# Optimization experiments

Hardware: AMD Instinct MI355X
Metric: run time of the kernel (lower is better)

Reference implementation:

```python
import jax, jax.numpy as jnp
import numpy as np

# ConvVAE2d config: img_size=64, kernel=stride=16 (same-padding -> 0 pad), non-overlapping patches
BS, CH, IMG, K, NC, HID, LAT = 1024, 3, 64, 16, 10, 1024, 128
OH = IMG // K          # patches per side = 4
L = OH * OH            # patches per image = 16
PD = CH * K * K        # flattened patch dim = 768


def setup_inputs() -> dict:
    key = jax.random.key(0)
    ks = jax.random.split(key, 8)
    def w(k_, shape, fan_in):
        return jax.random.normal(k_, shape, dtype=jnp.float32) * np.float32(1.0 / np.sqrt(fan_in))
    return {
        "x": jax.random.uniform(ks[0], (BS, CH, IMG, IMG), dtype=jnp.float32),
        "c": jax.random.uniform(ks[1], (BS, NC), dtype=jnp.float32),
        # cvae_small.encode params: [patch++class] -> hidden -> 2*latent
        "enc_w1": w(ks[2], (PD + NC, HID), PD + NC),
        "enc_b1": jnp.zeros((HID,), jnp.float32),
        "enc_w2": w(ks[3], (HID, 2 * LAT), HID),
        "enc_b2": jnp.zeros((2 * LAT,), jnp.float32),
        # cvae_small.decode params: [z++class] -> hidden -> patch (sigmoid)
        "dec_w1": w(ks[4], (LAT + NC, HID), LAT + NC),
        "dec_b1": jnp.zeros((HID,), jnp.float32),
        "dec_w2": w(ks[5], (HID, PD), HID),
        "dec_b2": jnp.zeros((PD,), jnp.float32),
    }


def reference(x, c, enc_w1, enc_b1, enc_w2, enc_b2, dec_w1, dec_b1, dec_w2, dec_b2):
    bs = x.shape[0]
    # --- encode_vae_layer: unfold into [bs, L, ch*k*k] patches (stride=k, pad=0) ---
    p = x.reshape(bs, CH, OH, K, OH, K).transpose(0, 2, 4, 1, 3, 5).reshape(bs, L, PD)
    cb = jnp.broadcast_to(c[:, None, :], (bs, L, NC))  # class vector per patch
    h = jax.nn.relu(jnp.concatenate([p, cb], axis=-1) @ enc_w1 + enc_b1)
    mu_logvar = h @ enc_w2 + enc_b2                    # [bs, L, 2*LAT]
    # --- reparameterize_vae_layer (deterministic=True -> z = mu) ---
    mu = mu_logvar[..., :LAT]
    # --- decode_vae_layer: per-patch decode, then fold back (non-overlapping) ---
    hd = jax.nn.relu(jnp.concatenate([mu, cb], axis=-1) @ dec_w1 + dec_b1)
    patches = jax.nn.sigmoid(hd @ dec_w2 + dec_b2)     # [bs, L, PD]
    recon = (patches.reshape(bs, OH, OH, CH, K, K)
                     .transpose(0, 3, 1, 4, 2, 5)
                     .reshape(bs, CH, IMG, IMG))
    # mu_logvar as a [bs, 2*latent, h/stride, w/stride] feature map
    mu_logvar_2d = mu_logvar.transpose(0, 2, 1).reshape(bs, 2 * LAT, OH, OH)
    return recon, mu_logvar_2d
```

## Files before the change

kernel.cpp:

```cpp
#include <hip/hip_runtime.h>

typedef unsigned short u16;
typedef unsigned int   u32;
typedef __bf16 bf16x8 __attribute__((ext_vector_type(8)));
typedef float  f32x4  __attribute__((ext_vector_type(4)));

__device__ __forceinline__ u16 f2b(float f) {
  u32 u = __builtin_bit_cast(u32, f);
  u = (u + 0x7fffu + ((u >> 16) & 1u)) >> 16;
  return (u16)u;
}
__device__ __forceinline__ float b2f(u16 h) {
  u32 u = ((u32)h) << 16;
  return __builtin_bit_cast(float, u);
}
__device__ __forceinline__ float ld_in(const void* p, size_t idx, int isf32) {
  return isf32 ? ((const float*)p)[idx] : b2f(((const u16*)p)[idx]);
}
__device__ __forceinline__ void async_cp16(const u16* g, u16* l) {
  __builtin_amdgcn_global_load_lds(
      (const __attribute__((address_space(1))) void*)g,
      (__attribute__((address_space(3))) void*)l, 16, 0, 0);
}

#define RECON_ELEMS 12582912

__global__ __launch_bounds__(256) void detect_f32(const u16* __restrict__ x,
                                                  int* __restrict__ flag) {
  __shared__ int s;
  if (threadIdx.x == 0) s = 0;
  __syncthreads();
  int bad = 0;
  for (int i = threadIdx.x; i < 2048; i += 256) {
    u16 u = x[i];
    if ((u & 0x8000u) || (u > 0x3F80u)) bad = 1;
  }
  if (bad) atomicOr(&s, 1);
  __syncthreads();
  if (threadIdx.x == 0) *flag = s;
}

__global__ __launch_bounds__(256) void build_a1(const void* __restrict__ x,
                                                const void* __restrict__ c,
                                                u16* __restrict__ A1,
                                                int R, int rowOff,
                                                const int* __restrict__ flag) {
  int g = blockIdx.x * 256 + threadIdx.x;
  if (g >= R * 112) return;
  int row = g / 112, grp = g - row * 112;
  int grow = row + rowOff;
  int b = grow >> 4, l = grow & 15, oh = l >> 2, ow = l & 3;
  int isf = *flag;
  u16* dst = &A1[(size_t)row * 896 + grp * 8];
  int col0 = grp * 8;
  if (col0 < 768) {
    int ch = col0 >> 8, kh = (col0 >> 4) & 15, kw = col0 & 15;
    size_t off = (size_t)b * 12288 + ch * 4096 + (oh * 16 + kh) * 64 + ow * 16 + kw;
    if (isf) {
      const float* s = (const float*)x + off;
      float4 f0 = *(const float4*)(s);
      float4 f1 = *(const float4*)(s + 4);
      dst[0] = f2b(f0.x); dst[1] = f2b(f0.y); dst[2] = f2b(f0.z); dst[3] = f2b(f0.w);
      dst[4] = f2b(f1.x); dst[5] = f2b(f1.y); dst[6] = f2b(f1.z); dst[7] = f2b(f1.w);
    } else {
      *(int4*)dst = *(const int4*)((const u16*)x + off);
    }
  } else {
#pragma unroll
    for (int t = 0; t < 8; ++t) {
      int col = col0 + t;
      dst[t] = (col < 778) ? f2b(ld_in(c, (size_t)b * 10 + (col - 768), isf)) : (u16)0;
    }
  }
}

__global__ __launch_bounds__(256) void prep_weights(const void* __restrict__ ew1,
                                                    const void* __restrict__ ew2,
                                                    const void* __restrict__ dw1,
                                                    const void* __restrict__ dw2,
                                                    u16* __restrict__ W1t,
                                                    u16* __restrict__ EW2t,
                                                    u16* __restrict__ W3t,
                                                    u16* __restrict__ DW2t,
                                                    const int* __restrict__ flag) {
  const int z = blockIdx.z;
  const void* src; u16* dst; int N, Kpad, Ksrc;
  if (z == 0)      { src = ew1; dst = W1t;  N = 1024; Kpad = 896;  Ksrc = 778;  }
  else if (z == 1) { src = ew2; dst = EW2t; N = 256;  Kpad = 1024; Ksrc = 1024; }
  else if (z == 2) { src = dw1; dst = W3t;  N = 1024; Kpad = 160;  Ksrc = 138;  }
  else             { src = dw2; dst = DW2t; N = 768;  Kpad = 1024; Ksrc = 1024; }
  const int k0 = blockIdx.x * 32, n0 = blockIdx.y * 32;
  if (k0 >= Kpad || n0 >= N) return;
  __shared__ float t[32][33];
  const int tx = threadIdx.x & 31, ty = threadIdx.x >> 5;
  const int isf = *flag;
#pragma unroll
  for (int j = 0; j < 4; ++j) {
    int k = k0 + ty + j * 8;
    t[ty + j * 8][tx] = (k < Ksrc) ? ld_in(src, (size_t)k * N + n0 + tx, isf) : 0.0f;
  }
  __syncthreads();
#pragma unroll
  for (int j = 0; j < 4; ++j) {
    int n = n0 + ty + j * 8;
    dst[(size_t)n * Kpad + k0 + tx] = f2b(t[tx][ty + j * 8]);
  }
}

template <int EPI>
__global__ __launch_bounds__(512, 2) void gemm_r3(const u16* __restrict__ A,
                                                  const u16* __restrict__ Bt,
                                                  const void* __restrict__ bias,
                                                  u16* __restrict__ outb,
                                                  float* __restrict__ outf,
                                                  int N, int K, int NBX, int NBY,
                                                  int rowOff,
                                                  const int* __restrict__ flag) {
  extern __shared__ __align__(16) u16 lds[];
  const int bid = blockIdx.x;
  const int xcd = bid & 7, idx = bid >> 3;
  const int byl = idx / NBX;
  const int by = xcd * (NBY >> 3) + byl;
  const int bx = idx - byl * NBX;
  const int rowBase = by * 256, colBase = bx * 256;

  const int tid = threadIdx.x;
  const int lane = tid & 63, w = tid >> 6;
  const int l16 = lane & 15, quad = lane >> 4;
  const int wm = w >> 2, wn = w & 3;
  const int swq = quad ^ ((l16 >> 1) & 3);

  const int isf = *flag;
  float bv[4];
#pragma unroll
  for (int nr = 0; nr < 4; ++nr)
    bv[nr] = ld_in(bias, colBase + wn * 64 + nr * 16 + l16, isf);
  asm volatile("s_waitcnt vmcnt(0)" ::: "memory");

  const int sA0 = tid, sA1 = tid + 512;
  const int rA0 = sA0 >> 2, qA0 = (sA0 & 3) ^ ((rA0 >> 1) & 3);
  const int rA1 = sA1 >> 2, qA1 = (sA1 & 3) ^ ((rA1 >> 1) & 3);
  const u16* gA0 = A  + (size_t)(rowBase + rA0) * K + qA0 * 8;
  const u16* gA1 = A  + (size_t)(rowBase + rA1) * K + qA1 * 8;
  const u16* gB0 = Bt + (size_t)(colBase + rA0) * K + qA0 * 8;
  const u16* gB1 = Bt + (size_t)(colBase + rA1) * K + qA1 * 8;

  f32x4 acc[8][4] = {};
  bf16x8 a[8], b[4];
  const int NT = K >> 5;

  async_cp16(gA0, lds + tid * 8);
  async_cp16(gA1, lds + 4096 + tid * 8);
  async_cp16(gB0, lds + 8192 + tid * 8);
  async_cp16(gB1, lds + 12288 + tid * 8);
  if (NT > 1) {
    u16* D = lds + 16384;
    async_cp16(gA0 + 32, D + tid * 8);
    async_cp16(gA1 + 32, D + 4096 + tid * 8);
    async_cp16(gB0 + 32, D + 8192 + tid * 8);
    async_cp16(gB1 + 32, D + 12288 + tid * 8);
    asm volatile("s_waitcnt vmcnt(4)" ::: "memory");
  } else {
    asm volatile("s_waitcnt vmcnt(0)" ::: "memory");
  }
  __builtin_amdgcn_s_barrier();

  int cur = 0;
  for (int t = 0; t < NT; ++t) {
    const u16* Lq = lds + cur * 16384;
#pragma unroll
    for (int mr = 0; mr < 8; ++mr)
      a[mr] = *(const bf16x8*)(Lq + (wm * 128 + mr * 16 + l16) * 32 + swq * 8);
#pragma unroll
    for (int nr = 0; nr < 4; ++nr)
      b[nr] = *(const bf16x8*)(Lq + 8192 + (wn * 64 + nr * 16 + l16) * 32 + swq * 8);
    if (t + 2 < NT) {
      const int d2 = (cur >= 1) ? cur - 1 : 2;
      u16* D = lds + d2 * 16384;
      const int ko = (t + 2) * 32;
      async_cp16(gA0 + ko, D + tid * 8);
      async_cp16(gA1 + ko, D + 4096 + tid * 8);
      async_cp16(gB0 + ko, D + 8192 + tid * 8);
      async_cp16(gB1 + ko, D + 12288 + tid * 8);
    }
    asm volatile("s_waitcnt lgkmcnt(0)" ::: "memory");
    __builtin_amdgcn_sched_barrier(0);
    __builtin_amdgcn_s_setprio(1);
#pragma unroll
    for (int mr = 0; mr < 8; ++mr)
#pragma unroll
      for (int nr = 0; nr < 4; ++nr)
        acc[mr][nr] = __builtin_amdgcn_mfma_f32_16x16x32_bf16(a[mr], b[nr], acc[mr][nr], 0, 0, 0);
    __builtin_amdgcn_s_setprio(0);
    __builtin_amdgcn_sched_barrier(0);
    if (t + 2 < NT)      asm volatile("s_waitcnt vmcnt(4)" ::: "memory");
    else if (t + 1 < NT) asm volatile("s_waitcnt vmcnt(0)" ::: "memory");
    if (t + 1 < NT) __builtin_amdgcn_s_barrier();
    cur = (cur >= 2) ? 0 : cur + 1;
  }

#pragma unroll
  for (int mr = 0; mr < 8; ++mr) {
    const int row0 = rowBase + wm * 128 + mr * 16 + quad * 4;
#pragma unroll
    for (int nr = 0; nr < 4; ++nr) {
      const int col = colBase + wn * 64 + nr * 16 + l16;
#pragma unroll
      for (int r = 0; r < 4; ++r) {
        const int row = row0 + r;
        float v = acc[mr][nr][r] + bv[nr];
        if (EPI == 0) {
          v = fmaxf(v, 0.0f);
          outb[(size_t)row * N + col] = f2b(v);
        } else {
          v = 1.0f / (1.0f + __expf(-v));
          const int grow = row + rowOff;
          const int bb = grow >> 4, l = grow & 15;
          const int oh = l >> 2, ow = l & 3;
          const int ch = col >> 8, kh = (col >> 4) & 15, kw = col & 15;
          outf[(size_t)bb * 12288 + ch * 4096 + (oh * 16 + kh) * 64 + ow * 16 + kw] = v;
        }
      }
    }
  }
}

__global__ __launch_bounds__(512, 2) void gemm_mid(u16* hio,
    const u16* __restrict__ EW2t, const u16* __restrict__ W3t,
    const void* __restrict__ c, const void* __restrict__ eb2,
    const void* __restrict__ db1, float* __restrict__ out2,
    int rowOff, const int* __restrict__ flag) {
  extern __shared__ __align__(16) u16 lds[];
  const int bid = blockIdx.x;
  const int lrowBase = bid * 64;
  const int growBase = rowOff + lrowBase;
  const int tid = threadIdx.x;
  const int lane = tid & 63, w = tid >> 6;
  const int l16 = lane & 15, quad = lane >> 4;
  const int swq = quad ^ ((l16 >> 1) & 3);
  const int wm = w >> 2, wn4 = w & 3;

  const int isf = *flag;
  float bv2[2], bv3[8][2];
#pragma unroll
  for (int nr = 0; nr < 2; ++nr)
    bv2[nr] = ld_in(eb2, w * 32 + nr * 16 + l16, isf);
#pragma unroll
  for (int np = 0; np < 8; ++np)
#pragma unroll
    for (int nr = 0; nr < 2; ++nr)
      bv3[np][nr] = ld_in(db1, np * 128 + wn4 * 32 + nr * 16 + l16, isf);
  asm volatile("s_waitcnt vmcnt(0)" ::: "memory");

  const int rA = tid >> 3, rcA = tid & 7;
  const int gcA = (rcA & 4) | ((rcA & 3) ^ ((rA >> 1) & 3));
  const u16* gAe = hio + (size_t)(lrowBase + rA) * 1024 + gcA * 8;
  const u16* gBe[4];
#pragma unroll
  for (int j = 0; j < 4; ++j) {
    const int sb = tid + j * 512;
    const int rB = sb >> 3, rcB = sb & 7;
    const int gcB = (rcB & 4) | ((rcB & 3) ^ ((rB >> 1) & 3));
    gBe[j] = EW2t + (size_t)rB * 1024 + gcB * 8;
  }

#define STGE(tt, s) do {                                                   \
    async_cp16(gAe + (tt) * 64, lds + (s) * 4096 + tid * 8);               \
    _Pragma("unroll") for (int j = 0; j < 4; ++j)                          \
      async_cp16(gBe[j] + (tt) * 64,                                       \
                 lds + 8192 + (s) * 16384 + (tid + j * 512) * 8);          \
  } while (0)

  f32x4 acce[4][2] = {};
  STGE(0, 0);
  int p = 0;
  for (int t = 0; t < 16; ++t) {
    if (t + 1 < 16) {
      STGE(t + 1, p ^ 1);
      asm volatile("s_waitcnt vmcnt(5)\n\ts_barrier" ::: "memory");
    } else {
      asm volatile("s_waitcnt vmcnt(0)\n\ts_barrier" ::: "memory");
    }
    const u16* AE = lds + p * 4096;
    const u16* BE = lds + 8192 + p * 16384;
    bf16x8 ae[4][2], be[2][2];
#pragma unroll
    for (int mr = 0; mr < 4; ++mr)
#pragma unroll
      for (int ks = 0; ks < 2; ++ks)
        ae[mr][ks] = *(const bf16x8*)(AE + (mr * 16 + l16) * 64 + ((ks * 4) | swq) * 8);
#pragma unroll
    for (int nr = 0; nr < 2; ++nr)
#pragma unroll
      for (int ks = 0; ks < 2; ++ks)
        be[nr][ks] = *(const bf16x8*)(BE + (w * 32 + nr * 16 + l16) * 64 + ((ks * 4) | swq) * 8);
    asm volatile("s_waitcnt lgkmcnt(0)" ::: "memory");
    __builtin_amdgcn_sched_barrier(0);
    __builtin_amdgcn_s_setprio(1);
#pragma unroll
    for (int mr = 0; mr < 4; ++mr)
#pragma unroll
      for (int nr = 0; nr < 2; ++nr)
#pragma unroll
        for (int ks = 0; ks < 2; ++ks)
          acce[mr][nr] = __builtin_amdgcn_mfma_f32_16x16x32_bf16(ae[mr][ks], be[nr][ks], acce[mr][nr], 0, 0, 0);
    __builtin_amdgcn_s_setprio(0);
    __builtin_amdgcn_sched_barrier(0);
    __builtin_amdgcn_s_barrier();
    p ^= 1;
  }
#undef STGE

  u16* A3 = lds + 40960;
#pragma unroll
  for (int mr = 0; mr < 4; ++mr)
#pragma unroll
    for (int nr = 0; nr < 2; ++nr) {
      const int col = w * 32 + nr * 16 + l16;
      const int row0 = mr * 16 + quad * 4;
#pragma unroll
      for (int r = 0; r < 4; ++r) {
        const int row = row0 + r;
        const int grow = growBase + row;
        const float v = acce[mr][nr][r] + bv2[nr];
        out2[(size_t)(grow >> 4) * 4096 + col * 16 + (grow & 15)] = v;
        if (col < 128) A3[row * 168 + col] = f2b(v);
      }
    }
  {
    const int rT = tid >> 3, cg = tid & 7;
    const int b = (growBase + rT) >> 4;
#pragma unroll
    for (int jj = 0; jj < 5; ++jj) {
      const int col = 128 + cg * 5 + jj;
      A3[rT * 168 + col] = (col < 138) ? f2b(ld_in(c, (size_t)b * 10 + col - 128, isf)) : (u16)0;
    }
  }
  asm volatile("s_waitcnt vmcnt(0) lgkmcnt(0)" ::: "memory");
  __builtin_amdgcn_s_barrier();

  int nW[5], cW[5];
#pragma unroll
  for (int j = 0; j < 5; ++j) {
    const int s5 = tid + j * 512;
    nW[j] = s5 / 20;
    cW[j] = s5 - nW[j] * 20;
  }
#pragma unroll
  for (int j = 0; j < 5; ++j)
    async_cp16(W3t + (size_t)nW[j] * 160 + cW[j] * 8, lds + (tid + j * 512) * 8);
  asm volatile("s_waitcnt vmcnt(0)" ::: "memory");
  __builtin_amdgcn_s_barrier();

  for (int np = 0; np < 8; ++np) {
    const int pb = np & 1;
    if (np < 7) {
#pragma unroll
      for (int j = 0; j < 5; ++j)
        async_cp16(W3t + (size_t)((np + 1) * 128 + nW[j]) * 160 + cW[j] * 8,
                   lds + (pb ^ 1) * 20480 + (tid + j * 512) * 8);
    }
    f32x4 accd[2][2] = {};
    const u16* WP = lds + pb * 20480;
#pragma unroll
    for (int t = 0; t < 5; ++t) {
      bf16x8 ad[2], bd[2];
#pragma unroll
      for (int mr = 0; mr < 2; ++mr)
        ad[mr] = *(const bf16x8*)(A3 + (wm * 32 + mr * 16 + l16) * 168 + (t * 4 + quad) * 8);
#pragma unroll
      for (int nr = 0; nr < 2; ++nr)
        bd[nr] = *(const bf16x8*)(WP + (wn4 * 32 + nr * 16 + l16) * 160 + (t * 4 + quad) * 8);
      asm volatile("s_waitcnt lgkmcnt(0)" ::: "memory");
      __builtin_amdgcn_sched_barrier(0);
#pragma unroll
      for (int mr = 0; mr < 2; ++mr)
#pragma unroll
        for (int nr = 0; nr < 2; ++nr)
          accd[mr][nr] = __builtin_amdgcn_mfma_f32_16x16x32_bf16(ad[mr], bd[nr], accd[mr][nr], 0, 0, 0);
    }
#pragma unroll
    for (int mr = 0; mr < 2; ++mr)
#pragma unroll
      for (int nr = 0; nr < 2; ++nr) {
        const int col = np * 128 + wn4 * 32 + nr * 16 + l16;
        const int row0 = wm * 32 + mr * 16 + quad * 4;
#pragma unroll
        for (int r = 0; r < 4; ++r) {
          const int row = row0 + r;
          const float v = fmaxf(accd[mr][nr][r] + bv3[np][nr], 0.0f);
          hio[(size_t)(lrowBase + row) * 1024 + col] = f2b(v);
        }
      }
    if (np < 7) {
      asm volatile("s_waitcnt vmcnt(16)" ::: "memory");
      __builtin_amdgcn_s_barrier();
    }
  }
}


extern "C" void kernel_launch(void* const* d_in, const int* in_sizes, int n_in,
                              void* d_out, int out_size, void* d_ws, size_t ws_size,
                              hipStream_t stream) {
  const void* x   = d_in[0];
  const void* c   = d_in[1];
  const void* ew1 = d_in[2];
  const void* eb1 = d_in[3];
  const void* ew2 = d_in[4];
  const void* eb2 = d_in[5];
  const void* dw1 = d_in[6];
  const void* db1 = d_in[7];
  const void* dw2 = d_in[8];
  const void* db2 = d_in[9];
  float* out  = (float*)d_out;
  u16*   ws   = (u16*)d_ws;

  static bool configured = false;
  if (!configured) {
    hipFuncSetAttribute(reinterpret_cast<const void*>(gemm_r3<0>),
                        hipFuncAttributeMaxDynamicSharedMemorySize, 98304);
    hipFuncSetAttribute(reinterpret_cast<const void*>(gemm_r3<2>),
                        hipFuncAttributeMaxDynamicSharedMemorySize, 98304);
    hipFuncSetAttribute(reinterpret_cast<const void*>(gemm_mid),
                        hipFuncAttributeMaxDynamicSharedMemorySize, 103424);
    configured = true;
  }

  const size_t fixedU16 = 8 + 917504 + 262144 + 163840 + 786432;
  int R = 2048;
  for (int cand = 16384; cand >= 2048; cand >>= 1) {
    if ((fixedU16 + (size_t)cand * 1920) * 2 <= ws_size) { R = cand; break; }
  }

  int* flag = (int*)ws;
  u16* W1t  = ws + 8;
  u16* EW2t = W1t + 917504;
  u16* W3t  = EW2t + 262144;
  u16* DW2t = W3t + 163840;
  u16* A1c  = DW2t + 786432;
  u16* hc   = A1c + (size_t)R * 896;
  float* out2 = out + RECON_ELEMS;

  detect_f32<<<dim3(1), dim3(256), 0, stream>>>((const u16*)x, flag);

  prep_weights<<<dim3(32, 32, 4), dim3(256), 0, stream>>>(ew1, ew2, dw1, dw2,
                                                          W1t, EW2t, W3t, DW2t, flag);

  const int chunks = 16384 / R;
  const int NBY = R / 256;
  for (int chunk = 0; chunk < chunks; ++chunk) {
    int rowOff = chunk * R;
    build_a1<<<dim3((R * 112 + 255) / 256), dim3(256), 0, stream>>>(x, c, A1c, R, rowOff, flag);
    gemm_r3<0><<<dim3(4 * NBY), dim3(512), 98304, stream>>>(A1c, W1t, eb1, hc, nullptr,
                                                            1024, 896, 4, NBY, rowOff, flag);
    gemm_mid<<<dim3(R / 64), dim3(512), 103424, stream>>>(hc, EW2t, W3t, c, eb2, db1,
                                                          out2, rowOff, flag);
    gemm_r3<2><<<dim3(3 * NBY), dim3(512), 98304, stream>>>(hc, DW2t, db2, nullptr, out,
                                                            768, 1024, 3, NBY, rowOff, flag);
  }
}
```

Baseline: 244.9 us.

## Fuse patch unfold into first GEMM's A-load via implicit-im2col addressing

Replaces the per-chunk build_a1 im2col kernel with a single cvt_x pass that converts x to bf16 in an image-major layout with the class vector appended. The first GEMM then computes patch addresses on the fly when staging A tiles. K is also reduced from 896 to 800 padding. This removes a materialized A1 buffer and trims padded MMA work, at the cost of extra address arithmetic and less contiguous A loads (16-element runs per patch row).

```diff
diff --git a/kernel.cpp b/kernel.cpp
--- a/kernel.cpp
+++ b/kernel.cpp
@@ -24,6 +24,7 @@
 }
 
 #define RECON_ELEMS 12582912
+#define XB_STRIDE 12544
 
 __global__ __launch_bounds__(256) void detect_f32(const u16* __restrict__ x,
                                                   int* __restrict__ flag) {
@@ -40,36 +41,35 @@
   if (threadIdx.x == 0) *flag = s;
 }
 
-__global__ __launch_bounds__(256) void build_a1(const void* __restrict__ x,
-                                                const void* __restrict__ c,
-                                                u16* __restrict__ A1,
-                                                int R, int rowOff,
-                                                const int* __restrict__ flag) {
-  int g = blockIdx.x * 256 + threadIdx.x;
-  if (g >= R * 112) return;
-  int row = g / 112, grp = g - row * 112;
-  int grow = row + rowOff;
-  int b = grow >> 4, l = grow & 15, oh = l >> 2, ow = l & 3;
-  int isf = *flag;
-  u16* dst = &A1[(size_t)row * 896 + grp * 8];
-  int col0 = grp * 8;
-  if (col0 < 768) {
-    int ch = col0 >> 8, kh = (col0 >> 4) & 15, kw = col0 & 15;
-    size_t off = (size_t)b * 12288 + ch * 4096 + (oh * 16 + kh) * 64 + ow * 16 + kw;
+__global__ __launch_bounds__(256) void cvt_x(const void* __restrict__ x,
+                                             const void* __restrict__ c,
+                                             u16* __restrict__ xb,
+                                             const int* __restrict__ flag) {
+  const int g = blockIdx.x * 256 + threadIdx.x;
+  const int isf = *flag;
+  if (g < 1572864) {
+    const size_t i = (size_t)g * 8;
+    const int b = (int)(i / 12288);
+    const int r = (int)(i - (size_t)b * 12288);
+    u16* dst = xb + (size_t)b * XB_STRIDE + r;
     if (isf) {
-      const float* s = (const float*)x + off;
+      const float* s = (const float*)x + i;
       float4 f0 = *(const float4*)(s);
       float4 f1 = *(const float4*)(s + 4);
       dst[0] = f2b(f0.x); dst[1] = f2b(f0.y); dst[2] = f2b(f0.z); dst[3] = f2b(f0.w);
       dst[4] = f2b(f1.x); dst[5] = f2b(f1.y); dst[6] = f2b(f1.z); dst[7] = f2b(f1.w);
     } else {
-      *(int4*)dst = *(const int4*)((const u16*)x + off);
-    }
-  } else {
-#pragma unroll
-    for (int t = 0; t < 8; ++t) {
-      int col = col0 + t;
-      dst[t] = (col < 778) ? f2b(ld_in(c, (size_t)b * 10 + (col - 768), isf)) : (u16)0;
+      *(int4*)dst = *(const int4*)((const u16*)x + i);
+    }
+  } else if (g < 1605632) {
+    const int t8 = g - 1572864;
+    const int b = t8 >> 5;
+    const int k8 = (t8 & 31) * 8;
+    u16* dst = xb + (size_t)b * XB_STRIDE + 12288 + k8;
+#pragma unroll
+    for (int j = 0; j < 8; ++j) {
+      const int col = k8 + j;
+      dst[j] = (col < 10) ? f2b(ld_in(c, (size_t)b * 10 + col, isf)) : (u16)0;
     }
   }
 }
@@ -85,7 +85,7 @@
                                                     const int* __restrict__ flag) {
   const int z = blockIdx.z;
   const void* src; u16* dst; int N, Kpad, Ksrc;
-  if (z == 0)      { src = ew1; dst = W1t;  N = 1024; Kpad = 896;  Ksrc = 778;  }
+  if (z == 0)      { src = ew1; dst = W1t;  N = 1024; Kpad = 800;  Ksrc = 778;  }
   else if (z == 1) { src = ew2; dst = EW2t; N = 256;  Kpad = 1024; Ksrc = 1024; }
   else if (z == 2) { src = dw1; dst = W3t;  N = 1024; Kpad = 160;  Ksrc = 138;  }
   else             { src = dw2; dst = DW2t; N = 768;  Kpad = 1024; Ksrc = 1024; }
@@ -107,7 +107,7 @@
   }
 }
 
-template <int EPI>
+template <int EPI, int AMODE>
 __global__ __launch_bounds__(512, 2) void gemm_r3(const u16* __restrict__ A,
                                                   const u16* __restrict__ Bt,
                                                   const void* __restrict__ bias,
@@ -140,25 +140,53 @@
   const int sA0 = tid, sA1 = tid + 512;
   const int rA0 = sA0 >> 2, qA0 = (sA0 & 3) ^ ((rA0 >> 1) & 3);
   const int rA1 = sA1 >> 2, qA1 = (sA1 & 3) ^ ((rA1 >> 1) & 3);
-  const u16* gA0 = A  + (size_t)(rowBase + rA0) * K + qA0 * 8;
-  const u16* gA1 = A  + (size_t)(rowBase + rA1) * K + qA1 * 8;
   const u16* gB0 = Bt + (size_t)(colBase + rA0) * K + qA0 * 8;
   const u16* gB1 = Bt + (size_t)(colBase + rA1) * K + qA1 * 8;
+  const u16* gA0 = nullptr; const u16* gA1 = nullptr;
+  int b1A0 = 0, b2A0 = 0, kq0 = 0, b1A1 = 0, b2A1 = 0, kq1 = 0;
+  if (AMODE == 0) {
+    gA0 = A + (size_t)(rowBase + rA0) * K + qA0 * 8;
+    gA1 = A + (size_t)(rowBase + rA1) * K + qA1 * 8;
+  } else {
+    const int g0 = rowOff + rowBase + rA0, g1 = rowOff + rowBase + rA1;
+    const int bb0 = g0 >> 4, ll0 = g0 & 15;
+    const int bb1 = g1 >> 4, ll1 = g1 & 15;
+    b1A0 = bb0 * XB_STRIDE + (ll0 >> 2) * 1024 + (ll0 & 3) * 16;
+    b1A1 = bb1 * XB_STRIDE + (ll1 >> 2) * 1024 + (ll1 & 3) * 16;
+    b2A0 = bb0 * XB_STRIDE + 11520;
+    b2A1 = bb1 * XB_STRIDE + 11520;
+    kq0 = qA0 * 8; kq1 = qA1 * 8;
+  }
+  auto aAddr = [&](int base1, int base2, int kq, int tt) -> const u16* {
+    const int k = kq + (tt << 5);
+    const int off = (k < 768)
+        ? base1 + ((k >> 8) << 12) + (((k >> 4) & 15) << 6) + (k & 15)
+        : base2 + k;
+    return A + off;
+  };
+#define STAGE_T(tt, D) do {                                                \
+    if (AMODE == 0) {                                                      \
+      const int ko_ = (tt) * 32;                                           \
+      async_cp16(gA0 + ko_, (D) + tid * 8);                                \
+      async_cp16(gA1 + ko_, (D) + 4096 + tid * 8);                         \
+    } else {                                                               \
+      async_cp16(aAddr(b1A0, b2A0, kq0, (tt)), (D) + tid * 8);             \
+      async_cp16(aAddr(b1A1, b2A1, kq1, (tt)), (D) + 4096 + tid * 8);      \
+    }                                                                      \
+    {                                                                      \
+      const int ko_ = (tt) * 32;                                           \
+      async_cp16(gB0 + ko_, (D) + 8192 + tid * 8);                         \
+      async_cp16(gB1 + ko_, (D) + 12288 + tid * 8);                        \
+    }                                                                      \
+  } while (0)
 
   f32x4 acc[8][4] = {};
   bf16x8 a[8], b[4];
   const int NT = K >> 5;
 
-  async_cp16(gA0, lds + tid * 8);
-  async_cp16(gA1, lds + 4096 + tid * 8);
-  async_cp16(gB0, lds + 8192 + tid * 8);
-  async_cp16(gB1, lds + 12288 + tid * 8);
+  STAGE_T(0, lds);
   if (NT > 1) {
-    u16* D = lds + 16384;
-    async_cp16(gA0 + 32, D + tid * 8);
-    async_cp16(gA1 + 32, D + 4096 + tid * 8);
-    async_cp16(gB0 + 32, D + 8192 + tid * 8);
-    async_cp16(gB1 + 32, D + 12288 + tid * 8);
+    STAGE_T(1, lds + 16384);
     asm volatile("s_waitcnt vmcnt(4)" ::: "memory");
   } else {
     asm volatile("s_waitcnt vmcnt(0)" ::: "memory");
@@ -176,12 +204,7 @@
       b[nr] = *(const bf16x8*)(Lq + 8192 + (wn * 64 + nr * 16 + l16) * 32 + swq * 8);
     if (t + 2 < NT) {
       const int d2 = (cur >= 1) ? cur - 1 : 2;
-      u16* D = lds + d2 * 16384;
-      const int ko = (t + 2) * 32;
-      async_cp16(gA0 + ko, D + tid * 8);
-      async_cp16(gA1 + ko, D + 4096 + tid * 8);
-      async_cp16(gB0 + ko, D + 8192 + tid * 8);
-      async_cp16(gB1 + ko, D + 12288 + tid * 8);
+      STAGE_T(t + 2, lds + d2 * 16384);
     }
     asm volatile("s_waitcnt lgkmcnt(0)" ::: "memory");
     __builtin_amdgcn_sched_barrier(0);
@@ -198,6 +221,7 @@
     if (t + 1 < NT) __builtin_amdgcn_s_barrier();
     cur = (cur >= 2) ? 0 : cur + 1;
   }
+#undef STAGE_T
 
 #pragma unroll
   for (int mr = 0; mr < 8; ++mr) {
@@ -418,31 +442,33 @@
 
   static bool configured = false;
   if (!configured) {
-    hipFuncSetAttribute(reinterpret_cast<const void*>(gemm_r3<0>),
+    hipFuncSetAttribute(reinterpret_cast<const void*>(gemm_r3<0, 1>),
                         hipFuncAttributeMaxDynamicSharedMemorySize, 98304);
-    hipFuncSetAttribute(reinterpret_cast<const void*>(gemm_r3<2>),
+    hipFuncSetAttribute(reinterpret_cast<const void*>(gemm_r3<2, 0>),
                         hipFuncAttributeMaxDynamicSharedMemorySize, 98304);
     hipFuncSetAttribute(reinterpret_cast<const void*>(gemm_mid),
                         hipFuncAttributeMaxDynamicSharedMemorySize, 103424);
     configured = true;
   }
 
-  const size_t fixedU16 = 8 + 917504 + 262144 + 163840 + 786432;
+  const size_t fixedU16 = 8 + 819200 + 262144 + 163840 + 786432 + 12845056;
   int R = 2048;
   for (int cand = 16384; cand >= 2048; cand >>= 1) {
-    if ((fixedU16 + (size_t)cand * 1920) * 2 <= ws_size) { R = cand; break; }
+    if ((fixedU16 + (size_t)cand * 1024) * 2 <= ws_size) { R = cand; break; }
   }
 
   int* flag = (int*)ws;
   u16* W1t  = ws + 8;
-  u16* EW2t = W1t + 917504;
+  u16* EW2t = W1t + 819200;
   u16* W3t  = EW2t + 262144;
   u16* DW2t = W3t + 163840;
-  u16* A1c  = DW2t + 786432;
-  u16* hc   = A1c + (size_t)R * 896;
+  u16* xb   = DW2t + 786432;
+  u16* hc   = xb + 12845056;
   float* out2 = out + RECON_ELEMS;
 
   detect_f32<<<dim3(1), dim3(256), 0, stream>>>((const u16*)x, flag);
+
+  cvt_x<<<dim3(6272), dim3(256), 0, stream>>>(x, c, xb, flag);
 
   prep_weights<<<dim3(32, 32, 4), dim3(256), 0, stream>>>(ew1, ew2, dw1, dw2,
                                                           W1t, EW2t, W3t, DW2t, flag);
@@ -451,12 +477,11 @@
   const int NBY = R / 256;
   for (int chunk = 0; chunk < chunks; ++chunk) {
     int rowOff = chunk * R;
-    build_a1<<<dim3((R * 112 + 255) / 256), dim3(256), 0, stream>>>(x, c, A1c, R, rowOff, flag);
-    gemm_r3<0><<<dim3(4 * NBY), dim3(512), 98304, stream>>>(A1c, W1t, eb1, hc, nullptr,
-                                                            1024, 896, 4, NBY, rowOff, flag);
+    gemm_r3<0, 1><<<dim3(4 * NBY), dim3(512), 98304, stream>>>(xb, W1t, eb1, hc, nullptr,
+                                                               1024, 800, 4, NBY, rowOff, flag);
     gemm_mid<<<dim3(R / 64), dim3(512), 103424, stream>>>(hc, EW2t, W3t, c, eb2, db1,
                                                           out2, rowOff, flag);
-    gemm_r3<2><<<dim3(3 * NBY), dim3(512), 98304, stream>>>(hc, DW2t, db2, nullptr, out,
-                                                            768, 1024, 3, NBY, rowOff, flag);
-  }
-}
+    gemm_r3<2, 0><<<dim3(3 * NBY), dim3(512), 98304, stream>>>(hc, DW2t, db2, nullptr, out,
+                                                               768, 1024, 3, NBY, rowOff, flag);
+  }
+}
```

Measured after the change: 234.4 us. 4.3% less time.
